# Optimization experiments

Hardware: AMD Instinct MI355X
Metric: run time of the kernel (lower is better)

Reference implementation:

```python
import jax, jax.numpy as jnp
import numpy as np

B, A, T, C = 8, 16, 512, 256
H = 8
DH = C // H
HID = 4 * C


def setup_inputs() -> dict:
    key = jax.random.key(0)
    ks = jax.random.split(key, 16)
    s = 0.02
    return {
        "x": jax.random.normal(ks[0], (B, A, T, C), jnp.float32),
        "ln1_w": jnp.ones((C,), jnp.float32),
        "ln1_b": jnp.zeros((C,), jnp.float32),
        "qkv_w": jax.random.normal(ks[1], (C, 3 * C), jnp.float32) * s,
        "qkv_b": jnp.zeros((3 * C,), jnp.float32),
        "proj_w": jax.random.normal(ks[2], (C, C), jnp.float32) * s,
        "proj_b": jnp.zeros((C,), jnp.float32),
        "ln2_w": jnp.ones((C,), jnp.float32),
        "ln2_b": jnp.zeros((C,), jnp.float32),
        "fc_w": jax.random.normal(ks[3], (C, HID), jnp.float32) * s,
        "fc_b": jnp.zeros((HID,), jnp.float32),
        "fc2_w": jax.random.normal(ks[4], (HID, C), jnp.float32) * s,
        "fc2_b": jnp.zeros((C,), jnp.float32),
    }


def _layernorm(x, w, b, eps=1e-5):
    mu = jnp.mean(x, axis=-1, keepdims=True)
    var = jnp.var(x, axis=-1, keepdims=True)
    return (x - mu) * jax.lax.rsqrt(var + eps) * w + b


def reference(x, ln1_w, ln1_b, qkv_w, qkv_b, proj_w, proj_b,
              ln2_w, ln2_b, fc_w, fc_b, fc2_w, fc2_b):
    # pre-LN block; note: residuals branch off the *normalized* tensor,
    # exactly as in the source forward().
    xn = _layernorm(x, ln1_w, ln1_b)                       # (B,A,T,C)

    qkv = xn @ qkv_w + qkv_b                               # (B,A,T,3C)
    q, k, v = jnp.split(qkv, 3, axis=-1)
    # (B,A,T,C) -> (B,A,H,T,Dh)
    def heads(t):
        return t.reshape(B, A, T, H, DH).transpose(0, 1, 3, 2, 4)
    q, k, v = heads(q), heads(k), heads(v)

    att = jnp.einsum('bahtd,bahsd->bahts', q, k) / np.sqrt(DH).astype(np.float32)
    att = jax.nn.softmax(att, axis=-1)                     # (B,A,H,T,T)
    y = jnp.einsum('bahts,bahsd->bahtd', att, v)
    y = y.transpose(0, 1, 3, 2, 4).reshape(B, A, T, C)
    y = y @ proj_w + proj_b

    x2 = xn + y
    x2n = _layernorm(x2, ln2_w, ln2_b)
    h = jax.nn.gelu(x2n @ fc_w + fc_b, approximate=False)
    m = h @ fc2_w + fc2_b
    return x2n + m
```

## Files before the change

kernel.cpp:

```cpp
#include <hip/hip_runtime.h>

typedef unsigned short u16;
typedef __attribute__((ext_vector_type(8))) short s16x8;
typedef __attribute__((ext_vector_type(4))) float f32x4;

#define MFMA_BF16(a,b,c) __builtin_amdgcn_mfma_f32_16x16x32_bf16((a),(b),(c),0,0,0)

#define GLL(gp, lp) __builtin_amdgcn_global_load_lds( \
    (const __attribute__((address_space(1))) void*)(gp), \
    (__attribute__((address_space(3))) void*)(lp), 16, 0, 0)

#define PIPE_WAIT_BAR(N) do { \
  asm volatile("s_waitcnt vmcnt(" #N ")" ::: "memory"); \
  __builtin_amdgcn_sched_barrier(0); \
  __builtin_amdgcn_s_barrier(); \
  __builtin_amdgcn_sched_barrier(0); \
} while (0)

#define PIPE_BAR() do { \
  asm volatile("" ::: "memory"); \
  __builtin_amdgcn_sched_barrier(0); \
  __builtin_amdgcn_s_barrier(); \
  __builtin_amdgcn_sched_barrier(0); \
} while (0)

__device__ __forceinline__ float b2f(u16 s){
  union { unsigned u; float f; } v; v.u = ((unsigned)s) << 16; return v.f;
}
__device__ __forceinline__ u16 f2b(float x){
  union { float f; unsigned u; } v; v.f = x;
  unsigned u = v.u;
  return (u16)((u + 0x7FFFu + ((u >> 16) & 1u)) >> 16);
}
__device__ __forceinline__ u16 f2b_trunc(float x){
  union { float f; unsigned u; } v; v.f = x;
  return (u16)(v.u >> 16);
}

__device__ __forceinline__ float gelu_fast(float v){
  float av = fabsf(v) * 0.70710678118654752f;
  float t  = __builtin_amdgcn_rcpf(1.0f + 0.3275911f * av);
  float p  = ((((1.061405429f * t - 1.453152027f) * t + 1.421413741f) * t
               - 0.284496736f) * t + 0.254829592f) * t;
  float erfa = 1.0f - p * __expf(-av * av);
  return 0.5f * v * (1.0f + copysignf(erfa, v));
}

__global__ __launch_bounds__(256) void wconv_all(
    const float* __restrict__ w0, u16* __restrict__ t0,
    const float* __restrict__ w1, u16* __restrict__ t1,
    const float* __restrict__ w2, u16* __restrict__ t2,
    const float* __restrict__ w3, u16* __restrict__ t3)
{
  int bid = blockIdx.x;
  const float* w; u16* t; int K, N, base;
  if (bid < 768)        { w = w0; t = t0; K = 256;  N = 768;  base = bid; }
  else if (bid < 1024)  { w = w1; t = t1; K = 256;  N = 256;  base = bid - 768; }
  else if (bid < 2048)  { w = w2; t = t2; K = 256;  N = 1024; base = bid - 1024; }
  else                  { w = w3; t = t3; K = 1024; N = 256;  base = bid - 2048; }
  int idx = base * 256 + threadIdx.x;
  if (idx >= K * N) return;
  int k = idx / N, n = idx - k * N;
  t[(size_t)n * K + k] = f2b(w[idx]);
}

__global__ __launch_bounds__(256) void ln_f32(const float* __restrict__ in,
    const float* __restrict__ gam, const float* __restrict__ bet, u16* __restrict__ out)
{
  int wv = threadIdx.x >> 6, lane = threadIdx.x & 63;
  size_t row = (size_t)blockIdx.x * 4 + wv;
  float4 u = *(const float4*)(in + row * 256 + lane * 4);
  float s  = u.x + u.y + u.z + u.w;
  float s2 = u.x*u.x + u.y*u.y + u.z*u.z + u.w*u.w;
  #pragma unroll
  for (int off = 32; off; off >>= 1){
    s  += __shfl_xor(s, off);
    s2 += __shfl_xor(s2, off);
  }
  float mean = s * (1.0f/256.0f);
  float var  = s2 * (1.0f/256.0f) - mean*mean;
  float rs   = rsqrtf(var + 1e-5f);
  int c = lane * 4;
  float4 g4 = *(const float4*)(gam + c);
  float4 b4 = *(const float4*)(bet + c);
  ushort4 o;
  o.x = f2b((u.x - mean)*rs*g4.x + b4.x);
  o.y = f2b((u.y - mean)*rs*g4.y + b4.y);
  o.z = f2b((u.z - mean)*rs*g4.z + b4.z);
  o.w = f2b((u.w - mean)*rs*g4.w + b4.w);
  *(ushort4*)(out + row * 256 + c) = o;
}

template<int EPI, int NT>
__global__ __launch_bounds__(256) void gemm128(
    const u16* __restrict__ A, const u16* __restrict__ Bt, const float* __restrict__ bias,
    const u16* __restrict__ res, void* __restrict__ o0v, u16* __restrict__ o1, u16* __restrict__ o2,
    int N, int K)
{
  __shared__ __align__(16) u16 lds[24576];
  int tid = threadIdx.x;
  int w = tid >> 6, lane = tid & 63;
  int quad = lane >> 4, c = lane & 15;
  int bid = blockIdx.x;
  int x = bid & 7, j = bid >> 3;
  int nt = j % NT, mt = (j / NT) * 8 + x;
  int wm = (w >> 1) * 64, wn = (w & 1) * 64;
  const u16* Abase = A + (size_t)mt * 128 * K;
  const u16* Bbase = Bt + (size_t)nt * 128 * K;
  int m0 = tid & 127, jj0 = tid >> 7;
  f32x4 zero = {0.f, 0.f, 0.f, 0.f};
  f32x4 acc[4][4];
  #pragma unroll
  for (int mi = 0; mi < 4; mi++)
    #pragma unroll
    for (int ni = 0; ni < 4; ni++) acc[mi][ni] = zero;

  auto stage = [&](int buf, int k0){
    u16* base = &lds[buf * 8192];
    GLL(Abase + (size_t)m0 * K + k0 + jj0 * 8,       &base[tid * 8]);
    GLL(Abase + (size_t)m0 * K + k0 + (jj0 + 2) * 8, &base[2048 + tid * 8]);
    GLL(Bbase + (size_t)m0 * K + k0 + jj0 * 8,       &base[4096 + tid * 8]);
    GLL(Bbase + (size_t)m0 * K + k0 + (jj0 + 2) * 8, &base[6144 + tid * 8]);
  };
  auto compute = [&](int cb){
    const u16* Lb = &lds[cb * 8192];
    s16x8 af[4], bfr[4];
    #pragma unroll
    for (int mi = 0; mi < 4; mi++)
      af[mi] = *(const s16x8*)&Lb[(quad * 128 + wm + mi * 16 + c) * 8];
    #pragma unroll
    for (int ni = 0; ni < 4; ni++)
      bfr[ni] = *(const s16x8*)&Lb[4096 + (quad * 128 + wn + ni * 16 + c) * 8];
    #pragma unroll
    for (int mi = 0; mi < 4; mi++)
      #pragma unroll
      for (int ni = 0; ni < 4; ni++)
        acc[mi][ni] = MFMA_BF16(af[mi], bfr[ni], acc[mi][ni]);
  };

  stage(0, 0); stage(1, 32); stage(2, 64);
  int cur = 0;
  int k0 = 0;
  for (; k0 + 96 < K; k0 += 32){
    PIPE_WAIT_BAR(8);
    compute(cur);
    PIPE_BAR();
    stage(cur, k0 + 96);
    cur = (cur == 2) ? 0 : cur + 1;
  }
  PIPE_WAIT_BAR(8); compute(cur); cur = (cur == 2) ? 0 : cur + 1;
  PIPE_WAIT_BAR(4); compute(cur); cur = (cur == 2) ? 0 : cur + 1;
  PIPE_WAIT_BAR(0); compute(cur);

  const int LS  = 132;
  int rr = tid >> 3;
  int c7 = tid & 7;

  #pragma unroll
  for (int ch = 0; ch < 4; ch++){
    __syncthreads();
    if ((w >> 1) == (ch >> 1)){
      #pragma unroll
      for (int mi2 = 0; mi2 < 2; mi2++){
        int mi = (ch & 1) * 2 + mi2;
        #pragma unroll
        for (int ni = 0; ni < 4; ni++){
          int col = wn + ni * 16 + c;
          float bv = bias[nt * 128 + col];
          #pragma unroll
          for (int r = 0; r < 4; r++){
            int cr = mi2 * 16 + quad * 4 + r;
            float vv = acc[mi][ni][r] + bv;
            if (EPI == 0){
              int gcol = nt * 128 + col;
              if ((gcol >> 8) == 0) vv *= 0.17677669529663687f;
              lds[cr * LS + col] = f2b(vv);
            }
          }
        }
      }
    }
    __syncthreads();
    int row = mt * 128 + ch * 32 + rr;
    #pragma unroll
    for (int jj2 = 0; jj2 < 2; jj2++){
      int colL = c7 * 8 + jj2 * 64;
      uint4 val = *(const uint4*)&lds[rr * LS + colL];
      if (EPI == 0){
        int gcol = nt * 128 + colL;
        int which = gcol >> 8, ccc = gcol & 255;
        int hh = ccc >> 5, d = ccc & 31;
        int ba = row >> 9, t = row & 511;
        size_t idx = (((size_t)(ba * 8 + hh)) * 512 + t) * 32 + d;
        u16* dst = (which == 0) ? (u16*)o0v : ((which == 1) ? o1 : o2);
        *(uint4*)(dst + idx) = val;
      } else {
        *(uint4*)((u16*)o0v + (size_t)row * N + nt * 128 + colL) = val;
      }
    }
  }
}

__global__ __launch_bounds__(512, 4) void ffn_fused(
    const u16* __restrict__ x2n, const u16* __restrict__ fcT, const float* __restrict__ fcb,
    const u16* __restrict__ fc2T, const float* __restrict__ fc2b, float* __restrict__ out)
{
  __shared__ __align__(16) u16 lds[24576];
  int tid = threadIdx.x;
  int w = tid >> 6, lane = tid & 63;
  int quad = lane >> 4, c = lane & 15;
  int mt = blockIdx.x;
  const u16* Abase = x2n + (size_t)mt * 64 * 256;
  char* ldsc = (char*)lds;
  char* hl   = (char*)lds + 32768;

  #pragma unroll
  for (int i = 0; i < 4; i++){
    int ci = i * 512 + tid;
    int row = ci >> 5, slot = ci & 31;
    int glow = (slot * 16) ^ ((row & 7) << 4);
    GLL((const char*)Abase + row * 512 + glow, ldsc + ci * 16);
  }
  f32x4 zero = {0.f, 0.f, 0.f, 0.f};
  f32x4 acc2[4][2];
  #pragma unroll
  for (int mi = 0; mi < 4; mi++){ acc2[mi][0] = zero; acc2[mi][1] = zero; }
  PIPE_WAIT_BAR(0);

  for (int hc = 0; hc < 8; hc++){
    f32x4 acc1[4];
    #pragma unroll
    for (int mi = 0; mi < 4; mi++) acc1[mi] = zero;
    int n1 = hc * 128 + w * 16 + c;
    const u16* fb = fcT + (size_t)n1 * 256 + quad * 8;
    #pragma unroll
    for (int ks = 0; ks < 8; ks++){
      s16x8 bf1 = *(const s16x8*)(fb + ks * 32);
      #pragma unroll
      for (int mi = 0; mi < 4; mi++){
        int row = mi * 16 + c;
        int kb = (ks * 64 + quad * 16) ^ ((row & 7) << 4);
        s16x8 af = *(const s16x8*)(ldsc + row * 512 + kb);
        acc1[mi] = MFMA_BF16(af, bf1, acc1[mi]);
      }
    }
    __syncthreads();
    {
      int colc = w * 16 + c;
      float bv = fcb[hc * 128 + colc];
      #pragma unroll
      for (int mi = 0; mi < 4; mi++){
        #pragma unroll
        for (int r = 0; r < 4; r++){
          int row = mi * 16 + quad * 4 + r;
          int by = (colc * 2) ^ ((row & 15) << 4);
          *(u16*)(hl + row * 256 + by) = f2b(gelu_fast(acc1[mi][r] + bv));
        }
      }
    }
    __syncthreads();
    #pragma unroll
    for (int ks = 0; ks < 4; ks++){
      s16x8 ha[4], bf2[2];
      #pragma unroll
      for (int ni = 0; ni < 2; ni++){
        int n = w * 32 + ni * 16 + c;
        bf2[ni] = *(const s16x8*)(fc2T + (size_t)n * 1024 + hc * 128 + ks * 32 + quad * 8);
      }
      #pragma unroll
      for (int mi = 0; mi < 4; mi++){
        int row = mi * 16 + c;
        int kb = (ks * 64 + quad * 16) ^ ((row & 15) << 4);
        ha[mi] = *(const s16x8*)(hl + row * 256 + kb);
      }
      #pragma unroll
      for (int mi = 0; mi < 4; mi++){
        acc2[mi][0] = MFMA_BF16(ha[mi], bf2[0], acc2[mi][0]);
        acc2[mi][1] = MFMA_BF16(ha[mi], bf2[1], acc2[mi][1]);
      }
    }
  }

  #pragma unroll
  for (int ni = 0; ni < 2; ni++){
    int col = w * 32 + ni * 16 + c;
    float bv = fc2b[col];
    #pragma unroll
    for (int mi = 0; mi < 4; mi++){
      #pragma unroll
      for (int r = 0; r < 4; r++){
        int row = mi * 16 + quad * 4 + r;
        int by = (col * 2) ^ ((row & 7) << 4);
        u16 xv = *(const u16*)(ldsc + row * 512 + by);
        acc2[mi][ni][r] += bv + b2f(xv);
      }
    }
  }
  __syncthreads();

  float* ldsF = (float*)lds;
  const int LSO = 260;
  int orow = tid >> 5, oc = (tid & 31) * 4;
  #pragma unroll
  for (int ch = 0; ch < 4; ch++){
    #pragma unroll
    for (int ni = 0; ni < 2; ni++){
      #pragma unroll
      for (int r = 0; r < 4; r++){
        int crow = quad * 4 + r;
        ldsF[crow * LSO + w * 32 + ni * 16 + c] = acc2[ch][ni][r];
      }
    }
    __syncthreads();
    size_t rb = ((size_t)mt * 64 + ch * 16 + orow) * 256;
    *(float4*)(out + rb + oc)       = *(const float4*)&ldsF[orow * LSO + oc];
    *(float4*)(out + rb + oc + 128) = *(const float4*)&ldsF[orow * LSO + oc + 128];
    __syncthreads();
  }
}

__global__ __launch_bounds__(256) void proj_ln(
    const u16* __restrict__ A, const u16* __restrict__ Bt, const float* __restrict__ bias,
    const u16* __restrict__ res, const float* __restrict__ gam, const float* __restrict__ bet,
    u16* __restrict__ x2n)
{
  __shared__ __align__(16) u16 lds[20480];
  int tid = threadIdx.x;
  int w = tid >> 6, lane = tid & 63;
  int quad = lane >> 4, c = lane & 15;
  int mt = blockIdx.x;
  int wn = w * 64;
  const u16* Abase = A + (size_t)mt * 64 * 256;
  int an = tid & 63, aj = tid >> 6;
  f32x4 zero = {0.f, 0.f, 0.f, 0.f};
  f32x4 acc[4][4];
  #pragma unroll
  for (int mi = 0; mi < 4; mi++)
    #pragma unroll
    for (int ni = 0; ni < 4; ni++) acc[mi][ni] = zero;

  auto stage = [&](int buf, int k0){
    u16* base = &lds[buf * 10240];
    GLL(Abase + (size_t)an * 256 + k0 + aj * 8, &base[tid * 8]);
    #pragma unroll
    for (int i = 0; i < 4; i++){
      int ci = tid + i * 256;
      int n = ci & 255, jjb = ci >> 8;
      GLL(Bt + (size_t)n * 256 + k0 + jjb * 8, &base[2048 + ci * 8]);
    }
  };
  auto compute = [&](int cb){
    const u16* base = &lds[cb * 10240];
    s16x8 af[4], bfr[4];
    #pragma unroll
    for (int mi = 0; mi < 4; mi++)
      af[mi] = *(const s16x8*)&base[(quad * 64 + mi * 16 + c) * 8];
    #pragma unroll
    for (int ni = 0; ni < 4; ni++)
      bfr[ni] = *(const s16x8*)&base[2048 + (quad * 256 + wn + ni * 16 + c) * 8];
    #pragma unroll
    for (int mi = 0; mi < 4; mi++)
      #pragma unroll
      for (int ni = 0; ni < 4; ni++)
        acc[mi][ni] = MFMA_BF16(af[mi], bfr[ni], acc[mi][ni]);
  };

  stage(0, 0);
  int cur = 0;
  for (int k0 = 32; k0 < 256; k0 += 32){
    stage(cur ^ 1, k0);
    PIPE_WAIT_BAR(5);
    compute(cur);
    PIPE_BAR();
    cur ^= 1;
  }
  PIPE_WAIT_BAR(0);
  compute(cur);
  __syncthreads();

  #pragma unroll
  for (int ni = 0; ni < 4; ni++){
    int col = wn + ni * 16 + c;
    float bv = bias[col];
    #pragma unroll
    for (int mi = 0; mi < 4; mi++){
      #pragma unroll
      for (int r = 0; r < 4; r++){
        int rowL = mi * 16 + quad * 4 + r;
        size_t gidx = ((size_t)mt * 64 + rowL) * 256 + col;
        lds[rowL * 264 + col] = f2b(acc[mi][ni][r] + bv + b2f(res[gidx]));
      }
    }
  }
  __syncthreads();

  int rowL = tid >> 2, part = (tid & 3) * 64;
  float s = 0.f, s2 = 0.f;
  #pragma unroll
  for (int i = 0; i < 16; i++){
    ushort4 u = *(const ushort4*)&lds[rowL * 264 + part + i * 4];
    float v0 = b2f(u.x), v1 = b2f(u.y), v2 = b2f(u.z), v3 = b2f(u.w);
    s  += v0 + v1 + v2 + v3;
    s2 += v0*v0 + v1*v1 + v2*v2 + v3*v3;
  }
  s  += __shfl_xor(s, 1);  s  += __shfl_xor(s, 2);
  s2 += __shfl_xor(s2, 1); s2 += __shfl_xor(s2, 2);
  float mean = s * (1.0f/256.0f);
  float var  = s2 * (1.0f/256.0f) - mean*mean;
  float rs   = rsqrtf(var + 1e-5f);
  size_t orow = ((size_t)mt * 64 + rowL) * 256;
  #pragma unroll
  for (int i = 0; i < 16; i++){
    int col = part + i * 4;
    ushort4 u = *(const ushort4*)&lds[rowL * 264 + col];
    float4 g4 = *(const float4*)(gam + col);
    float4 b4 = *(const float4*)(bet + col);
    ushort4 o;
    o.x = f2b((b2f(u.x) - mean)*rs*g4.x + b4.x);
    o.y = f2b((b2f(u.y) - mean)*rs*g4.y + b4.y);
    o.z = f2b((b2f(u.z) - mean)*rs*g4.z + b4.z);
    o.w = f2b((b2f(u.w) - mean)*rs*g4.w + b4.w);
    *(ushort4*)(x2n + orow + col) = o;
  }
}

__global__ __launch_bounds__(256) void attn_kernel(const u16* __restrict__ q,
    const u16* __restrict__ k, const u16* __restrict__ v, u16* __restrict__ y)
{
  __shared__ __align__(16) u16 ldsK[32 * 36];
  __shared__ __align__(16) u16 ldsV[32 * 36];
  __shared__ __align__(16) u16 ldsp[4][16 * 36];
  int tid = threadIdx.x;
  int w = tid >> 6, lane = tid & 63;
  int quad = lane >> 4, c = lane & 15;
  int bid = blockIdx.x;
  int x = bid & 7, j = bid >> 3;
  int qt = j & 3, bah = (j >> 2) * 8 + x;
  int q0 = qt * 128 + w * 32;
  const u16* qb = q + (size_t)bah * 16384;
  const u16* kb = k + (size_t)bah * 16384;
  const u16* vb = v + (size_t)bah * 16384;
  int krow = tid >> 3, kcol = (tid & 7) * 4;
  int vd = tid & 31,  vs = (tid >> 5) * 4;

  s16x8 qf0 = *(const s16x8*)(qb + (q0 + c) * 32 + quad * 8);
  s16x8 qf1 = *(const s16x8*)(qb + (q0 + 16 + c) * 32 + quad * 8);
  float l0[4] = {0.f,0.f,0.f,0.f}, l1[4] = {0.f,0.f,0.f,0.f};
  f32x4 o00 = {0,0,0,0}, o01 = {0,0,0,0}, o10 = {0,0,0,0}, o11 = {0,0,0,0};
  f32x4 zero = {0,0,0,0};

  for (int s0 = 0; s0 < 512; s0 += 32){
    uint2 kr = *(const uint2*)(kb + (s0 + krow) * 32 + kcol);
    short4 vr;
    vr.x = (short)vb[(s0 + vs)     * 32 + vd];
    vr.y = (short)vb[(s0 + vs + 1) * 32 + vd];
    vr.z = (short)vb[(s0 + vs + 2) * 32 + vd];
    vr.w = (short)vb[(s0 + vs + 3) * 32 + vd];
    __syncthreads();
    *(uint2*)&ldsK[krow * 36 + kcol] = kr;
    *(short4*)&ldsV[vd * 36 + vs]   = vr;
    __syncthreads();

    s16x8 kf0 = *(const s16x8*)&ldsK[c * 36 + quad * 8];
    s16x8 kf1 = *(const s16x8*)&ldsK[(16 + c) * 36 + quad * 8];
    s16x8 vf0 = *(const s16x8*)&ldsV[c * 36 + quad * 8];
    s16x8 vf1 = *(const s16x8*)&ldsV[(16 + c) * 36 + quad * 8];

    f32x4 S0 = MFMA_BF16(qf0, kf0, zero);
    f32x4 S1 = MFMA_BF16(qf0, kf1, zero);
    #pragma unroll
    for (int r = 0; r < 4; r++){
      float p0 = __expf(S0[r]), p1 = __expf(S1[r]);
      l0[r] += p0 + p1;
      int prow = quad * 4 + r;
      ldsp[w][prow * 36 + c]      = f2b_trunc(p0);
      ldsp[w][prow * 36 + 16 + c] = f2b_trunc(p1);
    }
    s16x8 pf = *(const s16x8*)&ldsp[w][c * 36 + quad * 8];
    o00 = MFMA_BF16(pf, vf0, o00);
    o01 = MFMA_BF16(pf, vf1, o01);

    S0 = MFMA_BF16(qf1, kf0, zero);
    S1 = MFMA_BF16(qf1, kf1, zero);
    #pragma unroll
    for (int r = 0; r < 4; r++){
      float p0 = __expf(S0[r]), p1 = __expf(S1[r]);
      l1[r] += p0 + p1;
      int prow = quad * 4 + r;
      ldsp[w][prow * 36 + c]      = f2b_trunc(p0);
      ldsp[w][prow * 36 + 16 + c] = f2b_trunc(p1);
    }
    pf = *(const s16x8*)&ldsp[w][c * 36 + quad * 8];
    o10 = MFMA_BF16(pf, vf0, o10);
    o11 = MFMA_BF16(pf, vf1, o11);
  }

  #pragma unroll
  for (int r = 0; r < 4; r++){
    #pragma unroll
    for (int off = 8; off; off >>= 1){
      l0[r] += __shfl_xor(l0[r], off);
      l1[r] += __shfl_xor(l1[r], off);
    }
  }

  int ba = bah >> 3, hh = bah & 7;
  #pragma unroll
  for (int r = 0; r < 4; r++){
    int t0 = q0 + quad * 4 + r;
    float inv0 = 1.0f / l0[r], inv1 = 1.0f / l1[r];
    size_t base0 = ((size_t)(ba * 512 + t0)) * 256 + hh * 32;
    size_t base1 = base0 + 16 * 256;
    y[base0 + c]      = f2b(o00[r] * inv0);
    y[base0 + 16 + c] = f2b(o01[r] * inv0);
    y[base1 + c]      = f2b(o10[r] * inv1);
    y[base1 + 16 + c] = f2b(o11[r] * inv1);
  }
}

extern "C" void kernel_launch(void* const* d_in, const int* in_sizes, int n_in,
                              void* d_out, int out_size, void* d_ws, size_t ws_size,
                              hipStream_t stream)
{
  const float* x      = (const float*)d_in[0];
  const float* ln1_w  = (const float*)d_in[1];
  const float* ln1_b  = (const float*)d_in[2];
  const float* qkv_w  = (const float*)d_in[3];
  const float* qkv_b  = (const float*)d_in[4];
  const float* proj_w = (const float*)d_in[5];
  const float* proj_b = (const float*)d_in[6];
  const float* ln2_w  = (const float*)d_in[7];
  const float* ln2_b  = (const float*)d_in[8];
  const float* fc_w   = (const float*)d_in[9];
  const float* fc_b   = (const float*)d_in[10];
  const float* fc2_w  = (const float*)d_in[11];
  const float* fc2_b  = (const float*)d_in[12];
  float* out = (float*)d_out;
  char* ws = (char*)d_ws;

  u16* xn   = (u16*)ws;
  u16* qb   = (u16*)(ws + (size_t)33554432);
  u16* kb   = qb + 16777216;
  u16* vb   = kb + 16777216;
  u16* yb   = vb + 16777216;
  u16* x2n  = (u16*)(ws + (size_t)173015040);
  u16* wqkvT  = (u16*)(ws + (size_t)206569472);
  u16* wprojT = wqkvT + 196608;
  u16* wfcT   = wprojT + 65536;
  u16* wfc2T  = wfcT + 262144;

  wconv_all<<<3072, 256, 0, stream>>>(qkv_w, wqkvT, proj_w, wprojT, fc_w, wfcT, fc2_w, wfc2T);

  ln_f32<<<16384, 256, 0, stream>>>(x, ln1_w, ln1_b, xn);
  gemm128<0,6><<<3072, 256, 0, stream>>>(xn, wqkvT, qkv_b, nullptr, qb, kb, vb, 768, 256);
  attn_kernel<<<4096, 256, 0, stream>>>(qb, kb, vb, yb);
  proj_ln<<<1024, 256, 0, stream>>>(yb, wprojT, proj_b, xn, ln2_w, ln2_b, x2n);
  ffn_fused<<<1024, 512, 0, stream>>>(x2n, wfcT, fc_b, wfc2T, fc2_b, out);
}
```

Measured before the change: 488.6 us.

## Double-buffer FFN hidden tile to overlap GEMM1 of next chunk with GEMM2

The FFN kernel now keeps two LDS buffers for the GELU hidden tile, so GEMM1 for chunk hc+1 runs alongside GEMM2 for chunk hc. This cuts the two barriers per iteration down to one. GEMM1 swaps its MFMA operands so each lane holds four consecutive hidden columns and can write them as one packed short4 store with a vectorized bias load. The cost is 16 KB more LDS per block, which may lower occupancy, plus more register pressure from overlapping the two GEMMs.

```diff
diff --git a/kernel.cpp b/kernel.cpp
--- a/kernel.cpp
+++ b/kernel.cpp
@@ -205,14 +205,15 @@
     const u16* __restrict__ x2n, const u16* __restrict__ fcT, const float* __restrict__ fcb,
     const u16* __restrict__ fc2T, const float* __restrict__ fc2b, float* __restrict__ out)
 {
-  __shared__ __align__(16) u16 lds[24576];
+  __shared__ __align__(16) u16 lds[32768];
   int tid = threadIdx.x;
   int w = tid >> 6, lane = tid & 63;
   int quad = lane >> 4, c = lane & 15;
   int mt = blockIdx.x;
   const u16* Abase = x2n + (size_t)mt * 64 * 256;
   char* ldsc = (char*)lds;
-  char* hl   = (char*)lds + 32768;
+  char* h0   = (char*)lds + 32768;
+  char* h1   = (char*)lds + 49152;
 
   #pragma unroll
   for (int i = 0; i < 4; i++){
@@ -227,12 +228,11 @@
   for (int mi = 0; mi < 4; mi++){ acc2[mi][0] = zero; acc2[mi][1] = zero; }
   PIPE_WAIT_BAR(0);
 
-  for (int hc = 0; hc < 8; hc++){
+  auto gemm1 = [&](int hcx, char* hw){
     f32x4 acc1[4];
     #pragma unroll
     for (int mi = 0; mi < 4; mi++) acc1[mi] = zero;
-    int n1 = hc * 128 + w * 16 + c;
-    const u16* fb = fcT + (size_t)n1 * 256 + quad * 8;
+    const u16* fb = fcT + (size_t)(hcx * 128 + w * 16 + c) * 256 + quad * 8;
     #pragma unroll
     for (int ks = 0; ks < 8; ks++){
       s16x8 bf1 = *(const s16x8*)(fb + ks * 32);
@@ -241,44 +241,50 @@
         int row = mi * 16 + c;
         int kb = (ks * 64 + quad * 16) ^ ((row & 7) << 4);
         s16x8 af = *(const s16x8*)(ldsc + row * 512 + kb);
-        acc1[mi] = MFMA_BF16(af, bf1, acc1[mi]);
-      }
-    }
-    __syncthreads();
-    {
-      int colc = w * 16 + c;
-      float bv = fcb[hc * 128 + colc];
-      #pragma unroll
-      for (int mi = 0; mi < 4; mi++){
-        #pragma unroll
-        for (int r = 0; r < 4; r++){
-          int row = mi * 16 + quad * 4 + r;
-          int by = (colc * 2) ^ ((row & 15) << 4);
-          *(u16*)(hl + row * 256 + by) = f2b(gelu_fast(acc1[mi][r] + bv));
-        }
-      }
-    }
-    __syncthreads();
+        acc1[mi] = MFMA_BF16(bf1, af, acc1[mi]);
+      }
+    }
+    float4 bb = *(const float4*)(fcb + hcx * 128 + w * 16 + quad * 4);
+    #pragma unroll
+    for (int mi = 0; mi < 4; mi++){
+      int m = mi * 16 + c;
+      short4 pk;
+      pk.x = (short)f2b(gelu_fast(acc1[mi][0] + bb.x));
+      pk.y = (short)f2b(gelu_fast(acc1[mi][1] + bb.y));
+      pk.z = (short)f2b(gelu_fast(acc1[mi][2] + bb.z));
+      pk.w = (short)f2b(gelu_fast(acc1[mi][3] + bb.w));
+      int by = (w * 32 + quad * 8) ^ ((m & 15) << 4);
+      *(short4*)(hw + m * 256 + by) = pk;
+    }
+  };
+  auto gemm2 = [&](int hcx, const char* hr){
     #pragma unroll
     for (int ks = 0; ks < 4; ks++){
-      s16x8 ha[4], bf2[2];
+      s16x8 bf2[2];
       #pragma unroll
       for (int ni = 0; ni < 2; ni++){
         int n = w * 32 + ni * 16 + c;
-        bf2[ni] = *(const s16x8*)(fc2T + (size_t)n * 1024 + hc * 128 + ks * 32 + quad * 8);
+        bf2[ni] = *(const s16x8*)(fc2T + (size_t)n * 1024 + hcx * 128 + ks * 32 + quad * 8);
       }
       #pragma unroll
       for (int mi = 0; mi < 4; mi++){
-        int row = mi * 16 + c;
-        int kb = (ks * 64 + quad * 16) ^ ((row & 15) << 4);
-        ha[mi] = *(const s16x8*)(hl + row * 256 + kb);
-      }
-      #pragma unroll
-      for (int mi = 0; mi < 4; mi++){
-        acc2[mi][0] = MFMA_BF16(ha[mi], bf2[0], acc2[mi][0]);
-        acc2[mi][1] = MFMA_BF16(ha[mi], bf2[1], acc2[mi][1]);
-      }
-    }
+        int m = mi * 16 + c;
+        int kb = (ks * 64 + quad * 16) ^ ((m & 15) << 4);
+        s16x8 ha = *(const s16x8*)(hr + m * 256 + kb);
+        acc2[mi][0] = MFMA_BF16(ha, bf2[0], acc2[mi][0]);
+        acc2[mi][1] = MFMA_BF16(ha, bf2[1], acc2[mi][1]);
+      }
+    }
+  };
+
+  gemm1(0, h0);
+  __syncthreads();
+  for (int hc = 0; hc < 8; hc++){
+    const char* hr = (hc & 1) ? h1 : h0;
+    char* hw       = (hc & 1) ? h0 : h1;
+    if (hc < 7) gemm1(hc + 1, hw);
+    gemm2(hc, hr);
+    __syncthreads();
   }
 
   #pragma unroll
```

After: 471.7 us. 3.5% less time.
